# Kernel tuning notes

Hardware: AMD Instinct MI355X
Metric: run time of the kernel (lower is better)

## Reference

```python
import jax, jax.numpy as jnp
import numpy as np
from jax import lax

G = 8      # deform groups (weight groups == offset groups)
K = 3      # kernel size
K2 = K * K


def conv3x3(x, w, b):
    # NCHW, 3x3, stride 1, padding 1 (SAME)
    y = lax.conv_general_dilated(x, w, (1, 1), 'SAME',
                                 dimension_numbers=('NCHW', 'OIHW', 'NCHW'))
    return y + b[None, :, None, None]


def deform_conv2d(ref, offsets, w, b):
    # ref: [B,C,H,W], offsets: [B,2*G*K2,H,W] (torchvision layout: per group,
    # per kernel position, (dy, dx) pairs), w: [C_out, C_in/G, K, K], b: [C_out]
    B, C, H, W = ref.shape
    Cg = C // G
    off = offsets.reshape(B, G, K2, 2, H, W)
    dy = off[:, :, :, 0]  # [B,G,K2,H,W]
    dx = off[:, :, :, 1]
    ky = (jnp.arange(K2) // K - K // 2).astype(ref.dtype)  # kernel y offsets (pad=1)
    kx = (jnp.arange(K2) % K - K // 2).astype(ref.dtype)
    base_y = jnp.arange(H, dtype=ref.dtype)[:, None] + ky[:, None, None]  # [K2,H,1]
    base_x = jnp.arange(W, dtype=ref.dtype)[None, :] + kx[:, None, None]  # [K2,1,W]
    py = dy + base_y  # [B,G,K2,H,W]
    px = dx + base_x

    y0 = jnp.floor(py).astype(jnp.int32)
    x0 = jnp.floor(px).astype(jnp.int32)
    ly = py - y0.astype(ref.dtype)
    lx = px - x0.astype(ref.dtype)

    ref_flat = ref.reshape(B, G, Cg, H * W)

    def gather(yi, xi):
        valid = (yi >= 0) & (yi < H) & (xi >= 0) & (xi < W)
        idx = jnp.clip(yi, 0, H - 1) * W + jnp.clip(xi, 0, W - 1)  # [B,G,K2,H,W]
        vals = jnp.take_along_axis(ref_flat, idx.reshape(B, G, 1, K2 * H * W), axis=3)
        vals = vals.reshape(B, G, Cg, K2, H, W)
        return vals * valid[:, :, None].astype(ref.dtype)

    w00 = ((1 - ly) * (1 - lx))[:, :, None]
    w01 = ((1 - ly) * lx)[:, :, None]
    w10 = (ly * (1 - lx))[:, :, None]
    w11 = (ly * lx)[:, :, None]
    sampled = (w00 * gather(y0, x0) + w01 * gather(y0, x0 + 1)
               + w10 * gather(y0 + 1, x0) + w11 * gather(y0 + 1, x0 + 1))
    # grouped accumulation: weight [C_out, Cg, K, K] -> [G, OCg, Cg, K2]
    wg = w.reshape(G, C // G, Cg, K2)
    out = jnp.einsum('bgikhw,goik->bgohw', sampled, wg)
    return out.reshape(B, C, H, W) + b[None, :, None, None]


def setup_inputs() -> dict:
    key = jax.random.key(0)
    ks = jax.random.split(key, 10)
    B, C, H, W = 2, 64, 256, 256
    s64 = 1.0 / np.sqrt(C * 9)
    s128 = 1.0 / np.sqrt(128 * 9)
    return {
        'offset': jax.random.normal(ks[0], (B, C, H, W), jnp.float32),
        'ref': jax.random.normal(ks[1], (B, C, H, W), jnp.float32),
        'w_off': jax.random.normal(ks[2], (2 * K2 * G, C, K, K), jnp.float32) * s64,
        'b_off': jnp.zeros((2 * K2 * G,), jnp.float32),
        'w_def': jax.random.normal(ks[3], (C, C // G, K, K), jnp.float32) * (1.0 / np.sqrt((C // G) * 9)),
        'b_def': jnp.zeros((C,), jnp.float32),
        'w_r1': jax.random.normal(ks[4], (C, 2 * C, K, K), jnp.float32) * s128,
        'b_r1': jnp.zeros((C,), jnp.float32),
        'w_r2': jax.random.normal(ks[5], (C, C, K, K), jnp.float32) * s64,
        'b_r2': jnp.zeros((C,), jnp.float32),
    }


def reference(offset, ref, w_off, b_off, w_def, b_def, w_r1, b_r1, w_r2, b_r2):
    deform_offsets = conv3x3(offset, w_off, b_off)              # [B,144,H,W]
    aligned_ref = deform_conv2d(ref, deform_offsets, w_def, b_def)
    x = jnp.concatenate([ref, aligned_ref], axis=1)             # [B,128,H,W]
    x = jax.nn.relu(conv3x3(x, w_r1, b_r1))
    x = jax.nn.relu(conv3x3(x, w_r2, b_r2))
    return x + aligned_ref
```

## Files before the change

### kernel.cpp

```cpp
#include <hip/hip_runtime.h>

typedef __attribute__((ext_vector_type(8))) short short8;
typedef __attribute__((ext_vector_type(4))) float float4v;

constexpr int HH = 256, WW = 256;
constexpr int PD = 258;
constexpr size_t HWsz = (size_t)HH * WW;

__device__ inline unsigned short f2bf(float f) {
    unsigned int u = __builtin_bit_cast(unsigned int, f);
    u += 0x7FFFu + ((u >> 16) & 1u);
    return (unsigned short)(u >> 16);
}
__device__ inline float bfhalf(unsigned int w, int hi) {
    return __builtin_bit_cast(float, hi ? (w & 0xFFFF0000u) : (w << 16));
}

template<int CDST, bool WRITE_G>
__global__ __launch_bounds__(256) void nchw_to_nhwc(
    const float* __restrict__ src, unsigned short* __restrict__ dst,
    unsigned short* __restrict__ dst_g)
{
    const int px = threadIdx.x, h = blockIdx.x, bi = blockIdx.y;
    const float* s = src + (size_t)bi * 64 * HWsz + (size_t)h * WW + px;
    unsigned short* d = dst + (((size_t)bi * PD + (h + 1)) * PD + (px + 1)) * CDST;
#pragma unroll
    for (int cg = 0; cg < 8; ++cg) {
        float v[8];
#pragma unroll
        for (int j = 0; j < 8; ++j) v[j] = s[(size_t)(cg * 8 + j) * HWsz];
        uint4 pk;
        pk.x = f2bf(v[0]) | ((unsigned)f2bf(v[1]) << 16);
        pk.y = f2bf(v[2]) | ((unsigned)f2bf(v[3]) << 16);
        pk.z = f2bf(v[4]) | ((unsigned)f2bf(v[5]) << 16);
        pk.w = f2bf(v[6]) | ((unsigned)f2bf(v[7]) << 16);
        *(uint4*)&d[cg * 8] = pk;
        if (WRITE_G) {
            unsigned short* dg = dst_g +
                (((size_t)(bi * 8 + cg) * HWsz) + (size_t)h * WW + px) * 8;
            *(uint4*)dg = pk;
        }
    }
}

__global__ __launch_bounds__(256) void pack_w(
    const float* __restrict__ w, short* __restrict__ wpk,
    int Cout, int Cin, int nElems)
{
    int e = blockIdx.x * 256 + threadIdx.x;
    if (e >= nElems) return;
    int j = e & 7;
    int lane = (e >> 3) & 63;
    int ksp = 9 * (Cin / 32);
    int kstep = (e >> 9) % ksp;
    int cot = (e >> 9) / ksp;
    int tap = kstep / (Cin / 32);
    int ci = (kstep % (Cin / 32)) * 32 + (lane >> 4) * 8 + j;
    int co = cot * 16 + (lane & 15);
    float v = (co < Cout) ? w[((size_t)co * Cin + ci) * 9 + tap] : 0.f;
    wpk[e] = (short)f2bf(v);
}

template<int CIN, int MODE, int COTB>
__global__ __launch_bounds__(256) void conv_mfma(
    const unsigned short* __restrict__ src,
    const short* __restrict__ wpk,
    const float* __restrict__ bias,
    unsigned short* __restrict__ dst_bf,
    float* __restrict__ dst_f,
    const float* __restrict__ resid)
{
    constexpr int KSTEPS = 9 * (CIN / 32);
    constexpr int CHUNKS = CIN / 64;

    __shared__ unsigned short lds[3 * 130 * 64];

    const int tid = threadIdx.x;
    const int lane = tid & 63;
    const int wv = tid >> 6;
    const int wy = wv >> 1;
    const int wx = wv & 1;
    const int quad = lane >> 4;
    const int nIdx = lane & 15;
    const int x0 = blockIdx.x * 128;
    const int h = blockIdx.y;
    const int bi = blockIdx.z / COTB;
    const int cb = blockIdx.z % COTB;
    const int coW = cb * 64 + wy * 32;

    const unsigned short* srcB = src + (size_t)bi * PD * PD * CIN;
    const short8* wbase = (const short8*)wpk;

    float4v acc[2][4];
#pragma unroll
    for (int af = 0; af < 2; ++af) {
        float4v b4;
#pragma unroll
        for (int r = 0; r < 4; ++r) {
            int co = coW + af * 16 + quad * 4 + r;
            float bv = 0.f;
            if (MODE != 0 || co < 144) bv = bias[co];
            b4[r] = bv;
        }
#pragma unroll
        for (int nt = 0; nt < 4; ++nt) acc[af][nt] = b4;
    }

    for (int ch = 0; ch < CHUNKS; ++ch) {
        __syncthreads();
        const unsigned short* g0 = srcB + ((size_t)h * PD + x0) * CIN + ch * 64;
#pragma unroll
        for (int r = 0; r < 3; ++r) {
            const unsigned short* grow = g0 + (size_t)r * PD * CIN;
            for (int q = tid; q < 1040; q += 256) {
                int px = q >> 3, cg = q & 7;
                uint4 v = *(const uint4*)(grow + (size_t)px * CIN + cg * 8);
                int ciSw = (cg * 8) ^ ((px & 7) << 3);
                *(uint4*)&lds[(r * 130 + px) * 64 + ciSw] = v;
            }
        }
        __syncthreads();

#pragma unroll
        for (int tap = 0; tap < 9; ++tap) {
            const int row = tap / 3, dxo = tap % 3;
#pragma unroll
            for (int s = 0; s < 2; ++s) {
                const int kstep = tap * (CIN / 32) + ch * 2 + s;
                short8 a0 = wbase[((size_t)(cb * 4 + wy * 2 + 0) * KSTEPS + kstep) * 64 + lane];
                short8 a1 = wbase[((size_t)(cb * 4 + wy * 2 + 1) * KSTEPS + kstep) * 64 + lane];
#pragma unroll
                for (int nt = 0; nt < 4; ++nt) {
                    int px = wx * 64 + nt * 16 + nIdx + dxo;
                    int ci = (s * 32 + quad * 8) ^ ((px & 7) << 3);
                    short8 b = *(const short8*)&lds[(row * 130 + px) * 64 + ci];
                    acc[0][nt] = __builtin_amdgcn_mfma_f32_16x16x32_bf16(a0, b, acc[0][nt], 0, 0, 0);
                    acc[1][nt] = __builtin_amdgcn_mfma_f32_16x16x32_bf16(a1, b, acc[1][nt], 0, 0, 0);
                }
            }
        }
    }

#pragma unroll
    for (int af = 0; af < 2; ++af) {
        const int co = coW + af * 16 + quad * 4;
#pragma unroll
        for (int nt = 0; nt < 4; ++nt) {
            const int px = x0 + wx * 64 + nt * 16 + nIdx;
            float4v a = acc[af][nt];
            if (MODE == 0) {
                if (co < 144) {
                    unsigned short* d = dst_bf + (size_t)bi * HWsz * 144;
                    uint2 pk;
                    pk.x = f2bf(a[0]) | ((unsigned)f2bf(a[1]) << 16);
                    pk.y = f2bf(a[2]) | ((unsigned)f2bf(a[3]) << 16);
                    *(uint2*)&d[((size_t)h * WW + px) * 144 + co] = pk;
                }
            } else if (MODE == 1) {
                unsigned short* d = dst_bf + (size_t)bi * PD * PD * 64;
                float v0 = fmaxf(a[0], 0.f), v1 = fmaxf(a[1], 0.f);
                float v2 = fmaxf(a[2], 0.f), v3 = fmaxf(a[3], 0.f);
                uint2 pk;
                pk.x = f2bf(v0) | ((unsigned)f2bf(v1) << 16);
                pk.y = f2bf(v2) | ((unsigned)f2bf(v3) << 16);
                *(uint2*)&d[(((size_t)h + 1) * PD + (px + 1)) * 64 + co] = pk;
            } else {
                float* d = dst_f + (size_t)bi * 64 * HWsz;
                const float* rs = resid + (size_t)bi * 64 * HWsz;
#pragma unroll
                for (int r = 0; r < 4; ++r) {
                    size_t idx = (size_t)(co + r) * HWsz + (size_t)h * WW + px;
                    d[idx] = fmaxf(a[r], 0.f) + rs[idx];
                }
            }
        }
    }
}

__global__ __launch_bounds__(256) void deform_k3(
    const unsigned short* __restrict__ refg,
    const unsigned short* __restrict__ doff,
    const float* __restrict__ wdef, const float* __restrict__ bdef,
    unsigned short* __restrict__ pcat_out,
    float* __restrict__ alignedf)
{
    __shared__ float wsm2[576];
    const int L = blockIdx.x;
    const int xcd = L & 7;
    const int j = L >> 3;
    const int g = j & 7;
    const int r = (j >> 3) & 31;
    const int bi = j >> 8;
    const int h = xcd * 32 + r;
    const int px = threadIdx.x;

    for (int i = threadIdx.x; i < 576; i += 256) {
        int o = i & 7, c = (i >> 3) & 7, k = i >> 6;
        wsm2[i] = wdef[(size_t)g * 576 + o * 72 + c * 9 + k];
    }
    __syncthreads();

    const unsigned int* dp = (const unsigned int*)(
        doff + (((size_t)bi * HWsz) + (size_t)h * WW + px) * 144 + g * 18);
    unsigned int dw[9];
#pragma unroll
    for (int k = 0; k < 9; ++k) dw[k] = dp[k];

    float acc[8];
#pragma unroll
    for (int o = 0; o < 8; ++o) acc[o] = bdef[g * 8 + o];

    const unsigned short* rb = refg + (size_t)(bi * 8 + g) * HWsz * 8;

#pragma unroll
    for (int k = 0; k < 9; ++k) {
        float dy = bfhalf(dw[k], 0);
        float dx = bfhalf(dw[k], 1);
        float py = dy + (float)(h + k / 3 - 1);
        float pxs = dx + (float)(px + k % 3 - 1);
        float fy = floorf(py), fx = floorf(pxs);
        int y0 = (int)fy, x0i = (int)fx;
        float ly = py - fy, lx = pxs - fx;
        int y1 = y0 + 1, x1i = x0i + 1;
        bool vy0 = (y0 >= 0) & (y0 < HH), vy1 = (y1 >= 0) & (y1 < HH);
        bool vx0 = (x0i >= 0) & (x0i < WW), vx1 = (x1i >= 0) & (x1i < WW);
        int cy0 = min(max(y0, 0), HH - 1), cy1 = min(max(y1, 0), HH - 1);
        int cx0 = min(max(x0i, 0), WW - 1), cx1 = min(max(x1i, 0), WW - 1);
        float w00 = (1.f - ly) * (1.f - lx), w01 = (1.f - ly) * lx;
        float w10 = ly * (1.f - lx), w11 = ly * lx;
        if (!(vy0 && vx0)) w00 = 0.f;
        if (!(vy0 && vx1)) w01 = 0.f;
        if (!(vy1 && vx0)) w10 = 0.f;
        if (!(vy1 && vx1)) w11 = 0.f;

        uint4 q00 = *(const uint4*)(rb + ((size_t)cy0 * WW + cx0) * 8);
        uint4 q01 = *(const uint4*)(rb + ((size_t)cy0 * WW + cx1) * 8);
        uint4 q10 = *(const uint4*)(rb + ((size_t)cy1 * WW + cx0) * 8);
        uint4 q11 = *(const uint4*)(rb + ((size_t)cy1 * WW + cx1) * 8);
        union U { uint4 v; unsigned int a[4]; };
        U u00{q00}, u01{q01}, u10{q10}, u11{q11};

#pragma unroll
        for (int cw = 0; cw < 4; ++cw) {
#pragma unroll
            for (int hl = 0; hl < 2; ++hl) {
                int c = cw * 2 + hl;
                float sv = w00 * bfhalf(u00.a[cw], hl) + w01 * bfhalf(u01.a[cw], hl)
                         + w10 * bfhalf(u10.a[cw], hl) + w11 * bfhalf(u11.a[cw], hl);
                const float* wp = &wsm2[((k * 8) + c) * 8];
                float4v wlo = *(const float4v*)wp;
                float4v whi = *(const float4v*)(wp + 4);
                acc[0] += wlo[0] * sv; acc[1] += wlo[1] * sv;
                acc[2] += wlo[2] * sv; acc[3] += wlo[3] * sv;
                acc[4] += whi[0] * sv; acc[5] += whi[1] * sv;
                acc[6] += whi[2] * sv; acc[7] += whi[3] * sv;
            }
        }
    }

    float* af = alignedf + ((size_t)(bi * 64 + g * 8)) * HWsz + (size_t)h * WW + px;
#pragma unroll
    for (int o = 0; o < 8; ++o) af[(size_t)o * HWsz] = acc[o];

    unsigned short* po = pcat_out + (((size_t)bi * PD + (h + 1)) * PD + (px + 1)) * 128 + 64 + g * 8;
    uint4 pk;
    pk.x = f2bf(acc[0]) | ((unsigned)f2bf(acc[1]) << 16);
    pk.y = f2bf(acc[2]) | ((unsigned)f2bf(acc[3]) << 16);
    pk.z = f2bf(acc[4]) | ((unsigned)f2bf(acc[5]) << 16);
    pk.w = f2bf(acc[6]) | ((unsigned)f2bf(acc[7]) << 16);
    *(uint4*)po = pk;
}

extern "C" void kernel_launch(void* const* d_in, const int* in_sizes, int n_in,
                              void* d_out, int out_size, void* d_ws, size_t ws_size,
                              hipStream_t stream)
{
    const float* offset = (const float*)d_in[0];
    const float* ref    = (const float*)d_in[1];
    const float* w_off  = (const float*)d_in[2];
    const float* b_off  = (const float*)d_in[3];
    const float* w_def  = (const float*)d_in[4];
    const float* b_def  = (const float*)d_in[5];
    const float* w_r1   = (const float*)d_in[6];
    const float* b_r1   = (const float*)d_in[7];
    const float* w_r2   = (const float*)d_in[8];
    const float* b_r2   = (const float*)d_in[9];
    float* out = (float*)d_out;

    unsigned short* p_off = (unsigned short*)d_ws;
    unsigned short* p_cat = p_off + (size_t)8520192;
    unsigned short* p_x1  = p_cat + (size_t)17040384;
    unsigned short* doff  = p_x1 + (size_t)8520192;
    unsigned short* refg  = doff + (size_t)18874368;
    float* alignedf = (float*)(refg + (size_t)8388608);
    short* wpk1  = (short*)(alignedf + (size_t)8388608);
    short* wpkr1 = wpk1 + 110592;
    short* wpkr2 = wpkr1 + 73728;

    hipMemsetAsync(d_ws, 0, (size_t)(8520192 + 17040384 + 8520192) * 2, stream);

    pack_w<<<dim3((110592 + 255) / 256), 256, 0, stream>>>(w_off, wpk1, 144, 64, 110592);
    pack_w<<<dim3((73728 + 255) / 256), 256, 0, stream>>>(w_r1, wpkr1, 64, 128, 73728);
    pack_w<<<dim3((36864 + 255) / 256), 256, 0, stream>>>(w_r2, wpkr2, 64, 64, 36864);

    nchw_to_nhwc<64, false><<<dim3(256, 2), 256, 0, stream>>>(offset, p_off, nullptr);
    nchw_to_nhwc<128, true><<<dim3(256, 2), 256, 0, stream>>>(ref, p_cat, refg);

    conv_mfma<64, 0, 3><<<dim3(2, 256, 6), 256, 0, stream>>>(
        p_off, wpk1, b_off, doff, nullptr, nullptr);

    deform_k3<<<dim3(4096), 256, 0, stream>>>(
        refg, doff, w_def, b_def, p_cat, alignedf);

    conv_mfma<128, 1, 1><<<dim3(2, 256, 2), 256, 0, stream>>>(
        p_cat, wpkr1, b_r1, p_x1, nullptr, nullptr);

    conv_mfma<64, 2, 1><<<dim3(2, 256, 2), 256, 0, stream>>>(
        p_x1, wpkr2, b_r2, nullptr, out, alignedf);
}
```

Measured before the change: 372.4 us.

## Switch convs to 32x32 MFMA full-row tiles, drop fp32 aligned buffer, zero borders only

The conv kernels move from 16x16x32 to 32x32x16 bf16 MFMA. Each block now covers a full 256-pixel row with 32-channel LDS chunks, a new weight packing and a new swizzle. The deform kernel no longer writes an fp32 aligned copy, and the final conv reads the residual from the bf16 concat buffer instead. That removes a large write and read but lowers the residual's precision to bf16. A small border-zeroing kernel replaces the full-workspace memset, and the deform inner loop is restructured into paired fma accumulators.

```diff
diff --git a/kernel.cpp b/kernel.cpp
--- a/kernel.cpp
+++ b/kernel.cpp
@@ -1,7 +1,8 @@
 #include <hip/hip_runtime.h>
 
-typedef __attribute__((ext_vector_type(8))) short short8;
-typedef __attribute__((ext_vector_type(4))) float float4v;
+typedef __attribute__((ext_vector_type(8)))  short  short8;
+typedef __attribute__((ext_vector_type(4)))  float  float4v;
+typedef __attribute__((ext_vector_type(16))) float  float16v;
 
 constexpr int HH = 256, WW = 256;
 constexpr int PD = 258;
@@ -14,6 +15,10 @@
 }
 __device__ inline float bfhalf(unsigned int w, int hi) {
     return __builtin_bit_cast(float, hi ? (w & 0xFFFF0000u) : (w << 16));
+}
+__device__ inline float2 unpk2(unsigned int u) {
+    return make_float2(__builtin_bit_cast(float, u << 16),
+                       __builtin_bit_cast(float, u & 0xFFFF0000u));
 }
 
 template<int CDST, bool WRITE_G>
@@ -43,7 +48,31 @@
     }
 }
 
-__global__ __launch_bounds__(256) void pack_w(
+__global__ __launch_bounds__(256) void zero_border(
+    unsigned short* __restrict__ p_off, unsigned short* __restrict__ p_cat,
+    unsigned short* __restrict__ p_x1)
+{
+    const int bi = blockIdx.y, which = blockIdx.z;
+    unsigned short* buf = which == 0 ? p_off : (which == 1 ? p_cat : p_x1);
+    const int CIN = (which == 1) ? 128 : 64;
+    const int NG = CIN / 8;
+    unsigned short* p = buf + (size_t)bi * PD * PD * CIN;
+    const int total = 1028 * 16;
+    for (int i = blockIdx.x * 256 + threadIdx.x; i < total; i += gridDim.x * 256) {
+        int g = i & 15;
+        if (g >= NG) continue;
+        int pxi = i >> 4;
+        int r, c;
+        if (pxi < 258)       { r = 0;   c = pxi; }
+        else if (pxi < 516)  { r = 257; c = pxi - 258; }
+        else if (pxi < 772)  { r = pxi - 516 + 1; c = 0; }
+        else                 { r = pxi - 772 + 1; c = 257; }
+        uint4 z = {0, 0, 0, 0};
+        *(uint4*)&p[((size_t)r * PD + c) * CIN + g * 8] = z;
+    }
+}
+
+__global__ __launch_bounds__(256) void pack_w32(
     const float* __restrict__ w, short* __restrict__ wpk,
     int Cout, int Cin, int nElems)
 {
@@ -51,72 +80,67 @@
     if (e >= nElems) return;
     int j = e & 7;
     int lane = (e >> 3) & 63;
-    int ksp = 9 * (Cin / 32);
+    int ksp = 9 * (Cin / 16);
     int kstep = (e >> 9) % ksp;
     int cot = (e >> 9) / ksp;
-    int tap = kstep / (Cin / 32);
-    int ci = (kstep % (Cin / 32)) * 32 + (lane >> 4) * 8 + j;
-    int co = cot * 16 + (lane & 15);
+    int tap = kstep / (Cin / 16);
+    int ci = (kstep % (Cin / 16)) * 16 + (lane >> 5) * 8 + j;
+    int co = cot * 32 + (lane & 31);
     float v = (co < Cout) ? w[((size_t)co * Cin + ci) * 9 + tap] : 0.f;
     wpk[e] = (short)f2bf(v);
 }
 
 template<int CIN, int MODE, int COTB>
-__global__ __launch_bounds__(256) void conv_mfma(
+__global__ __launch_bounds__(256, 2) void conv_mfma32(
     const unsigned short* __restrict__ src,
     const short* __restrict__ wpk,
     const float* __restrict__ bias,
     unsigned short* __restrict__ dst_bf,
     float* __restrict__ dst_f,
-    const float* __restrict__ resid)
-{
-    constexpr int KSTEPS = 9 * (CIN / 32);
-    constexpr int CHUNKS = CIN / 64;
-
-    __shared__ unsigned short lds[3 * 130 * 64];
-
-    const int tid = threadIdx.x;
+    const unsigned short* __restrict__ resid_bf)
+{
+    constexpr int CHUNKS = CIN / 32;
+    constexpr int KST = 9 * (CIN / 16);
+
+    __shared__ unsigned short lds[3 * 258 * 32];
+
+    const int tid  = threadIdx.x;
     const int lane = tid & 63;
-    const int wv = tid >> 6;
-    const int wy = wv >> 1;
-    const int wx = wv & 1;
-    const int quad = lane >> 4;
-    const int nIdx = lane & 15;
-    const int x0 = blockIdx.x * 128;
-    const int h = blockIdx.y;
-    const int bi = blockIdx.z / COTB;
-    const int cb = blockIdx.z % COTB;
-    const int coW = cb * 64 + wy * 32;
+    const int wv   = tid >> 6;
+    const int half = lane >> 5;
+    const int n32  = lane & 31;
+    const int h  = blockIdx.x;
+    const int bi = blockIdx.y / COTB;
+    const int cb = blockIdx.y % COTB;
 
     const unsigned short* srcB = src + (size_t)bi * PD * PD * CIN;
     const short8* wbase = (const short8*)wpk;
 
-    float4v acc[2][4];
-#pragma unroll
-    for (int af = 0; af < 2; ++af) {
-        float4v b4;
-#pragma unroll
-        for (int r = 0; r < 4; ++r) {
-            int co = coW + af * 16 + quad * 4 + r;
-            float bv = 0.f;
-            if (MODE != 0 || co < 144) bv = bias[co];
-            b4[r] = bv;
-        }
-#pragma unroll
-        for (int nt = 0; nt < 4; ++nt) acc[af][nt] = b4;
+    float16v acc[2][2];
+#pragma unroll
+    for (int coF = 0; coF < 2; ++coF) {
+        float16v bv;
+#pragma unroll
+        for (int reg = 0; reg < 16; ++reg) {
+            int co = cb * 64 + coF * 32 + (reg >> 2) * 8 + 4 * half + (reg & 3);
+            float b = 0.f;
+            if (MODE != 0 || co < 144) b = bias[co];
+            bv[reg] = b;
+        }
+        acc[coF][0] = bv;
+        acc[coF][1] = bv;
     }
 
     for (int ch = 0; ch < CHUNKS; ++ch) {
         __syncthreads();
-        const unsigned short* g0 = srcB + ((size_t)h * PD + x0) * CIN + ch * 64;
 #pragma unroll
         for (int r = 0; r < 3; ++r) {
-            const unsigned short* grow = g0 + (size_t)r * PD * CIN;
-            for (int q = tid; q < 1040; q += 256) {
-                int px = q >> 3, cg = q & 7;
-                uint4 v = *(const uint4*)(grow + (size_t)px * CIN + cg * 8);
-                int ciSw = (cg * 8) ^ ((px & 7) << 3);
-                *(uint4*)&lds[(r * 130 + px) * 64 + ciSw] = v;
+            const unsigned short* grow = srcB + ((size_t)(h + r) * PD) * CIN + ch * 32;
+            for (int q = tid; q < 1032; q += 256) {
+                int pc = q >> 2, g = q & 3;
+                uint4 v = *(const uint4*)(grow + (size_t)pc * CIN + g * 8);
+                int gsw = g ^ ((pc >> 1) & 3);
+                *(uint4*)&lds[((size_t)r * 258 + pc) * 32 + gsw * 8] = v;
             }
         }
         __syncthreads();
@@ -126,65 +150,69 @@
             const int row = tap / 3, dxo = tap % 3;
 #pragma unroll
             for (int s = 0; s < 2; ++s) {
-                const int kstep = tap * (CIN / 32) + ch * 2 + s;
-                short8 a0 = wbase[((size_t)(cb * 4 + wy * 2 + 0) * KSTEPS + kstep) * 64 + lane];
-                short8 a1 = wbase[((size_t)(cb * 4 + wy * 2 + 1) * KSTEPS + kstep) * 64 + lane];
-#pragma unroll
-                for (int nt = 0; nt < 4; ++nt) {
-                    int px = wx * 64 + nt * 16 + nIdx + dxo;
-                    int ci = (s * 32 + quad * 8) ^ ((px & 7) << 3);
-                    short8 b = *(const short8*)&lds[(row * 130 + px) * 64 + ci];
-                    acc[0][nt] = __builtin_amdgcn_mfma_f32_16x16x32_bf16(a0, b, acc[0][nt], 0, 0, 0);
-                    acc[1][nt] = __builtin_amdgcn_mfma_f32_16x16x32_bf16(a1, b, acc[1][nt], 0, 0, 0);
+                const int kstep = tap * (CIN / 16) + ch * 2 + s;
+                short8 a0 = wbase[((size_t)(cb * 2 + 0) * KST + kstep) * 64 + lane];
+                short8 a1 = wbase[((size_t)(cb * 2 + 1) * KST + kstep) * 64 + lane];
+#pragma unroll
+                for (int nt = 0; nt < 2; ++nt) {
+                    int pc = wv * 64 + nt * 32 + n32 + dxo;
+                    int gsw = (s * 2 + half) ^ ((pc >> 1) & 3);
+                    short8 b = *(const short8*)&lds[((size_t)row * 258 + pc) * 32 + gsw * 8];
+                    acc[0][nt] = __builtin_amdgcn_mfma_f32_32x32x16_bf16(a0, b, acc[0][nt], 0, 0, 0);
+                    acc[1][nt] = __builtin_amdgcn_mfma_f32_32x32x16_bf16(a1, b, acc[1][nt], 0, 0, 0);
                 }
             }
         }
     }
 
 #pragma unroll
-    for (int af = 0; af < 2; ++af) {
-        const int co = coW + af * 16 + quad * 4;
-#pragma unroll
-        for (int nt = 0; nt < 4; ++nt) {
-            const int px = x0 + wx * 64 + nt * 16 + nIdx;
-            float4v a = acc[af][nt];
-            if (MODE == 0) {
-                if (co < 144) {
-                    unsigned short* d = dst_bf + (size_t)bi * HWsz * 144;
+    for (int coF = 0; coF < 2; ++coF) {
+#pragma unroll
+        for (int nt = 0; nt < 2; ++nt) {
+            const int px = wv * 64 + nt * 32 + n32;
+            float16v a = acc[coF][nt];
+#pragma unroll
+            for (int q = 0; q < 4; ++q) {
+                const int co4 = cb * 64 + coF * 32 + q * 8 + 4 * half;
+                float v0 = a[q * 4 + 0], v1 = a[q * 4 + 1];
+                float v2 = a[q * 4 + 2], v3 = a[q * 4 + 3];
+                if (MODE == 0) {
+                    if (co4 < 144) {
+                        unsigned short* d = dst_bf + (size_t)bi * HWsz * 144;
+                        uint2 pk;
+                        pk.x = f2bf(v0) | ((unsigned)f2bf(v1) << 16);
+                        pk.y = f2bf(v2) | ((unsigned)f2bf(v3) << 16);
+                        *(uint2*)&d[((size_t)h * WW + px) * 144 + co4] = pk;
+                    }
+                } else if (MODE == 1) {
+                    unsigned short* d = dst_bf + (size_t)bi * PD * PD * 64;
                     uint2 pk;
-                    pk.x = f2bf(a[0]) | ((unsigned)f2bf(a[1]) << 16);
-                    pk.y = f2bf(a[2]) | ((unsigned)f2bf(a[3]) << 16);
-                    *(uint2*)&d[((size_t)h * WW + px) * 144 + co] = pk;
-                }
-            } else if (MODE == 1) {
-                unsigned short* d = dst_bf + (size_t)bi * PD * PD * 64;
-                float v0 = fmaxf(a[0], 0.f), v1 = fmaxf(a[1], 0.f);
-                float v2 = fmaxf(a[2], 0.f), v3 = fmaxf(a[3], 0.f);
-                uint2 pk;
-                pk.x = f2bf(v0) | ((unsigned)f2bf(v1) << 16);
-                pk.y = f2bf(v2) | ((unsigned)f2bf(v3) << 16);
-                *(uint2*)&d[(((size_t)h + 1) * PD + (px + 1)) * 64 + co] = pk;
-            } else {
-                float* d = dst_f + (size_t)bi * 64 * HWsz;
-                const float* rs = resid + (size_t)bi * 64 * HWsz;
-#pragma unroll
-                for (int r = 0; r < 4; ++r) {
-                    size_t idx = (size_t)(co + r) * HWsz + (size_t)h * WW + px;
-                    d[idx] = fmaxf(a[r], 0.f) + rs[idx];
+                    pk.x = f2bf(fmaxf(v0, 0.f)) | ((unsigned)f2bf(fmaxf(v1, 0.f)) << 16);
+                    pk.y = f2bf(fmaxf(v2, 0.f)) | ((unsigned)f2bf(fmaxf(v3, 0.f)) << 16);
+                    *(uint2*)&d[(((size_t)h + 1) * PD + (px + 1)) * 64 + co4] = pk;
+                } else {
+                    const unsigned short* rp = resid_bf + (size_t)bi * PD * PD * 128;
+                    uint2 rv = *(const uint2*)&rp[(((size_t)h + 1) * PD + (px + 1)) * 128 + 64 + co4];
+                    float r0 = bfhalf(rv.x, 0), r1 = bfhalf(rv.x, 1);
+                    float r2 = bfhalf(rv.y, 0), r3 = bfhalf(rv.y, 1);
+                    float* d = dst_f + (size_t)bi * 64 * HWsz + (size_t)h * WW + px;
+                    d[(size_t)(co4 + 0) * HWsz] = fmaxf(v0, 0.f) + r0;
+                    d[(size_t)(co4 + 1) * HWsz] = fmaxf(v1, 0.f) + r1;
+                    d[(size_t)(co4 + 2) * HWsz] = fmaxf(v2, 0.f) + r2;
+                    d[(size_t)(co4 + 3) * HWsz] = fmaxf(v3, 0.f) + r3;
                 }
             }
         }
     }
 }
 
-__global__ __launch_bounds__(256) void deform_k3(
+__global__ __launch_bounds__(256) void deform_k4(
     const unsigned short* __restrict__ refg,
     const unsigned short* __restrict__ doff,
     const float* __restrict__ wdef, const float* __restrict__ bdef,
-    unsigned short* __restrict__ pcat_out,
-    float* __restrict__ alignedf)
-{
-    __shared__ float wsm2[576];
+    unsigned short* __restrict__ pcat_out)
+{
+    __shared__ float2 wsm3[288];
     const int L = blockIdx.x;
     const int xcd = L & 7;
     const int j = L >> 3;
@@ -194,9 +222,10 @@
     const int h = xcd * 32 + r;
     const int px = threadIdx.x;
 
-    for (int i = threadIdx.x; i < 576; i += 256) {
-        int o = i & 7, c = (i >> 3) & 7, k = i >> 6;
-        wsm2[i] = wdef[(size_t)g * 576 + o * 72 + c * 9 + k];
+    for (int i = threadIdx.x; i < 288; i += 256) {
+        int o = i & 7, p = (i >> 3) & 3, k = i >> 5;
+        const float* wg = wdef + (size_t)g * 576 + o * 72;
+        wsm3[i] = make_float2(wg[(2 * p) * 9 + k], wg[(2 * p + 1) * 9 + k]);
     }
     __syncthreads();
 
@@ -206,9 +235,9 @@
 #pragma unroll
     for (int k = 0; k < 9; ++k) dw[k] = dp[k];
 
-    float acc[8];
-#pragma unroll
-    for (int o = 0; o < 8; ++o) acc[o] = bdef[g * 8 + o];
+    float2 acc2[8];
+#pragma unroll
+    for (int o = 0; o < 8; ++o) acc2[o] = make_float2(bdef[g * 8 + o], 0.f);
 
     const unsigned short* rb = refg + (size_t)(bi * 8 + g) * HWsz * 8;
 
@@ -241,33 +270,31 @@
         U u00{q00}, u01{q01}, u10{q10}, u11{q11};
 
 #pragma unroll
-        for (int cw = 0; cw < 4; ++cw) {
-#pragma unroll
-            for (int hl = 0; hl < 2; ++hl) {
-                int c = cw * 2 + hl;
-                float sv = w00 * bfhalf(u00.a[cw], hl) + w01 * bfhalf(u01.a[cw], hl)
-                         + w10 * bfhalf(u10.a[cw], hl) + w11 * bfhalf(u11.a[cw], hl);
-                const float* wp = &wsm2[((k * 8) + c) * 8];
-                float4v wlo = *(const float4v*)wp;
-                float4v whi = *(const float4v*)(wp + 4);
-                acc[0] += wlo[0] * sv; acc[1] += wlo[1] * sv;
-                acc[2] += wlo[2] * sv; acc[3] += wlo[3] * sv;
-                acc[4] += whi[0] * sv; acc[5] += whi[1] * sv;
-                acc[6] += whi[2] * sv; acc[7] += whi[3] * sv;
+        for (int p = 0; p < 4; ++p) {
+            float2 c00 = unpk2(u00.a[p]), c01 = unpk2(u01.a[p]);
+            float2 c10 = unpk2(u10.a[p]), c11 = unpk2(u11.a[p]);
+            float2 sv;
+            sv.x = fmaf(w00, c00.x, fmaf(w01, c01.x, fmaf(w10, c10.x, w11 * c11.x)));
+            sv.y = fmaf(w00, c00.y, fmaf(w01, c01.y, fmaf(w10, c10.y, w11 * c11.y)));
+            const float2* wp2 = &wsm3[((size_t)k * 4 + p) * 8];
+#pragma unroll
+            for (int o = 0; o < 8; ++o) {
+                acc2[o].x = fmaf(wp2[o].x, sv.x, acc2[o].x);
+                acc2[o].y = fmaf(wp2[o].y, sv.y, acc2[o].y);
             }
         }
     }
 
-    float* af = alignedf + ((size_t)(bi * 64 + g * 8)) * HWsz + (size_t)h * WW + px;
-#pragma unroll
-    for (int o = 0; o < 8; ++o) af[(size_t)o * HWsz] = acc[o];
+    float a[8];
+#pragma unroll
+    for (int o = 0; o < 8; ++o) a[o] = acc2[o].x + acc2[o].y;
 
     unsigned short* po = pcat_out + (((size_t)bi * PD + (h + 1)) * PD + (px + 1)) * 128 + 64 + g * 8;
     uint4 pk;
-    pk.x = f2bf(acc[0]) | ((unsigned)f2bf(acc[1]) << 16);
-    pk.y = f2bf(acc[2]) | ((unsigned)f2bf(acc[3]) << 16);
-    pk.z = f2bf(acc[4]) | ((unsigned)f2bf(acc[5]) << 16);
-    pk.w = f2bf(acc[6]) | ((unsigned)f2bf(acc[7]) << 16);
+    pk.x = f2bf(a[0]) | ((unsigned)f2bf(a[1]) << 16);
+    pk.y = f2bf(a[2]) | ((unsigned)f2bf(a[3]) << 16);
+    pk.z = f2bf(a[4]) | ((unsigned)f2bf(a[5]) << 16);
+    pk.w = f2bf(a[6]) | ((unsigned)f2bf(a[7]) << 16);
     *(uint4*)po = pk;
 }
 
@@ -292,29 +319,27 @@
     unsigned short* p_x1  = p_cat + (size_t)17040384;
     unsigned short* doff  = p_x1 + (size_t)8520192;
     unsigned short* refg  = doff + (size_t)18874368;
-    float* alignedf = (float*)(refg + (size_t)8388608);
-    short* wpk1  = (short*)(alignedf + (size_t)8388608);
+    short* wpk1  = (short*)(refg + (size_t)8388608);
     short* wpkr1 = wpk1 + 110592;
     short* wpkr2 = wpkr1 + 73728;
 
-    hipMemsetAsync(d_ws, 0, (size_t)(8520192 + 17040384 + 8520192) * 2, stream);
-
-    pack_w<<<dim3((110592 + 255) / 256), 256, 0, stream>>>(w_off, wpk1, 144, 64, 110592);
-    pack_w<<<dim3((73728 + 255) / 256), 256, 0, stream>>>(w_r1, wpkr1, 64, 128, 73728);
-    pack_w<<<dim3((36864 + 255) / 256), 256, 0, stream>>>(w_r2, wpkr2, 64, 64, 36864);
+    zero_border<<<dim3(65, 2, 3), 256, 0, stream>>>(p_off, p_cat, p_x1);
+
+    pack_w32<<<dim3((110592 + 255) / 256), 256, 0, stream>>>(w_off, wpk1, 144, 64, 110592);
+    pack_w32<<<dim3((73728 + 255) / 256), 256, 0, stream>>>(w_r1, wpkr1, 64, 128, 73728);
+    pack_w32<<<dim3((36864 + 255) / 256), 256, 0, stream>>>(w_r2, wpkr2, 64, 64, 36864);
 
     nchw_to_nhwc<64, false><<<dim3(256, 2), 256, 0, stream>>>(offset, p_off, nullptr);
     nchw_to_nhwc<128, true><<<dim3(256, 2), 256, 0, stream>>>(ref, p_cat, refg);
 
-    conv_mfma<64, 0, 3><<<dim3(2, 256, 6), 256, 0, stream>>>(
+    conv_mfma32<64, 0, 3><<<dim3(256, 6), 256, 0, stream>>>(
         p_off, wpk1, b_off, doff, nullptr, nullptr);
 
-    deform_k3<<<dim3(4096), 256, 0, stream>>>(
-        refg, doff, w_def, b_def, p_cat, alignedf);
-
-    conv_mfma<128, 1, 1><<<dim3(2, 256, 2), 256, 0, stream>>>(
+    deform_k4<<<dim3(4096), 256, 0, stream>>>(refg, doff, w_def, b_def, p_cat);
+
+    conv_mfma32<128, 1, 1><<<dim3(256, 2), 256, 0, stream>>>(
         p_cat, wpkr1, b_r1, p_x1, nullptr, nullptr);
 
-    conv_mfma<64, 2, 1><<<dim3(2, 256, 2), 256, 0, stream>>>(
-        p_x1, wpkr2, b_r2, nullptr, out, alignedf);
-}
+    conv_mfma32<64, 2, 1><<<dim3(256, 2), 256, 0, stream>>>(
+        p_x1, wpkr2, b_r2, nullptr, out, p_cat);
+}
```

Measured after the change: 398.2 us. 1.07x slower.
